# Kernel optimization log

Measured on AMD Instinct MI355X. Metric: run time of the kernel, lower is better.

Reference implementation:

```python
import jax, jax.numpy as jnp
import numpy as np

B, T, N = 128, 4096, 48  # batch, seq_len, num NER tags


def setup_inputs() -> dict:
    key = jax.random.key(0)
    k1, k2, k3, k4, k5 = jax.random.split(key, 5)
    return {
        "emissions": jax.random.normal(k1, (B, T, N), dtype=jnp.float32) * 0.01,
        "transitions": jax.random.normal(k2, (N, N), dtype=jnp.float32) * 0.01,
        "start": jax.random.normal(k3, (N,), dtype=jnp.float32) * 0.01,
        "end": jax.random.normal(k4, (N,), dtype=jnp.float32) * 0.01,
        "tags": jax.random.randint(k5, (B, T), 0, N, dtype=jnp.int32),
    }


def _crf_nll(emissions, transitions, start, end, tags):
    # --- forward_partition: log Z via forward algorithm (logsumexp recursion) ---
    em_t = jnp.transpose(emissions, (1, 0, 2))  # [T, B, N]
    alpha0 = start[None, :] + em_t[0]           # dp[0][j] = start(j) + emit(0, j)

    def step(alpha, em):
        # alpha: [B, N] over previous tag y_; transitions[y_, y]
        new = jax.nn.logsumexp(alpha[:, :, None] + transitions[None, :, :], axis=1) + em
        return new, None

    alpha_T, _ = jax.lax.scan(step, alpha0, em_t[1:])  # [B, N]
    log_Z = jax.nn.logsumexp(alpha_T + end[None, :], axis=-1)  # [B]

    # --- score_seq: gold-path score ---
    em_score = jnp.take_along_axis(emissions, tags[:, :, None], axis=2)[:, :, 0].sum(axis=1)
    trans_score = transitions[tags[:, :-1], tags[:, 1:]].sum(axis=1)
    score = start[tags[:, 0]] + em_score + trans_score + end[tags[:, -1]]

    return log_Z - score  # per-sequence NLL, [B]


def reference(emissions, transitions, start, end, tags):
    return _crf_nll(emissions, transitions, start, end, tags)
```

## Files before the change

### kernel.cpp

```cpp
#include <hip/hip_runtime.h>
#include <cmath>

#define BB 128
#define TT 4096
#define NN 48

typedef short bf16x8 __attribute__((ext_vector_type(8)));
typedef float f32x4 __attribute__((ext_vector_type(4)));
typedef float v2f   __attribute__((ext_vector_type(2)));
typedef int   i32x4 __attribute__((ext_vector_type(4)));
typedef int   i32x2 __attribute__((ext_vector_type(2)));

__device__ __forceinline__ float wave_reduce_sum(float v) {
  #pragma unroll
  for (int m = 32; m >= 1; m >>= 1) v += __shfl_xor(v, m, 64);
  return v;
}
__device__ __forceinline__ int bperm(int byteidx, int src) {
  return __builtin_amdgcn_ds_bpermute(byteidx, src);
}
__device__ __forceinline__ float lane_bcast(float x, int lane) {
  return __uint_as_float((unsigned)__builtin_amdgcn_readlane(__float_as_int(x), lane));
}
__device__ __forceinline__ int cvt_pk_bf16(float lo, float hi) {
  int r;
  asm("v_cvt_pk_bf16_f32 %0, %1, %2" : "=v"(r) : "v"(lo), "v"(hi));
  return r;
}
__device__ __forceinline__ unsigned short f2bf(float f) {
  unsigned u = __float_as_uint(f);
  unsigned r = (u + 0x7FFFu + ((u >> 16) & 1u)) >> 16;
  return (unsigned short)r;
}

template<int NC, int CL>
__launch_bounds__(64, 2)
__global__ void crf_chunk_kernel(const float* __restrict__ em,
                                 const float* __restrict__ trans,
                                 const int* __restrict__ tags,
                                 unsigned short* __restrict__ G,
                                 float* __restrict__ sc_part) {
  const int blk = blockIdx.x;
  const int b = blk / NC;
  const int c = blk % NC;
  const int l = threadIdx.x;
  const int g = l >> 4;
  const int rr = l & 15;
  const int jc = (l < NN) ? l : (NN - 1);
  const float FSCALE = 1.0f / 48.0f;

  bf16x8 Af0[3], Af1[3];
  #pragma unroll
  for (int mt = 0; mt < 3; ++mt) {
    const int i = 16 * mt + rr;
    bf16x8 a0, a1;
    #pragma unroll
    for (int e = 0; e < 8; ++e) {
      int k0 = 16 * (e >> 2) + 4 * g + (e & 3);
      a0[e] = (short)f2bf(__expf(trans[k0 * NN + i]) * FSCALE);
      int k1 = 32 + 4 * g + e;
      a1[e] = (e < 4) ? (short)f2bf(__expf(trans[k1 * NN + i]) * FSCALE) : (short)0;
    }
    Af0[mt] = a0; Af1[mt] = a1;
  }

  int pk0[3][3], pk1[3][3];
  #pragma unroll
  for (int mt = 0; mt < 3; ++mt)
  #pragma unroll
  for (int nt = 0; nt < 3; ++nt) {
    int r0 = 16 * mt + 4 * g, col = 16 * nt + rr;
    pk0[mt][nt] = ((r0     == col) ? 0x3F80 : 0) | (((r0 + 1 == col) ? 0x3F80 : 0) << 16);
    pk1[mt][nt] = ((r0 + 2 == col) ? 0x3F80 : 0) | (((r0 + 3 == col) ? 0x3F80 : 0) << 16);
  }

  const float* embr = em + (size_t)b * TT * NN + jc;
  const int t0 = c * CL + 1;
  const int count = (c == NC - 1) ? (CL - 1) : CL;
  const int wbase = g << 4;

  float pf0 = embr[(size_t)(t0 + 0) * NN];
  float pf1 = embr[(size_t)(t0 + 1) * NN];
  float pf2 = embr[(size_t)(t0 + 2) * NN];
  float pf3 = embr[(size_t)(t0 + 3) * NN];

  #define STEP(PF, NEXT_T) do {                                               \
    float w_ = __expf(PF);                                                    \
    int nt_ = (NEXT_T) > (TT - 1) ? (TT - 1) : (NEXT_T);                      \
    PF = embr[(size_t)nt_ * NN];                                              \
    int wi_ = __float_as_int(w_);                                             \
    v2f wv_[3][2];                                                            \
    _Pragma("unroll") for (int mt = 0; mt < 3; ++mt)                          \
    _Pragma("unroll") for (int h = 0; h < 2; ++h) {                           \
      int wa = bperm(wbase + mt * 64 + (2 * h) * 4, wi_);                     \
      int wb = bperm(wbase + mt * 64 + (2 * h + 1) * 4, wi_);                 \
      v2f t; t.x = __uint_as_float((unsigned)wa);                             \
      t.y = __uint_as_float((unsigned)wb); wv_[mt][h] = t;                    \
    }                                                                         \
    i32x4 B0v[3], B1v[3];                                                     \
    _Pragma("unroll") for (int nt = 0; nt < 3; ++nt) {                        \
      i32x4 b0; b0[0]=pk0[0][nt]; b0[1]=pk1[0][nt]; b0[2]=pk0[1][nt]; b0[3]=pk1[1][nt]; \
      i32x4 b1; b1[0]=pk0[2][nt]; b1[1]=pk1[2][nt]; b1[2]=0; b1[3]=0;         \
      B0v[nt] = b0; B1v[nt] = b1;                                             \
    }                                                                         \
    f32x4 acc_[3][3];                                                         \
    _Pragma("unroll") for (int mt = 0; mt < 3; ++mt)                          \
    _Pragma("unroll") for (int nt = 0; nt < 3; ++nt) {                        \
      f32x4 z = {0.f, 0.f, 0.f, 0.f};                                         \
      z = __builtin_amdgcn_mfma_f32_16x16x32_bf16(                            \
            Af0[mt], __builtin_bit_cast(bf16x8, B0v[nt]), z, 0, 0, 0);        \
      z = __builtin_amdgcn_mfma_f32_16x16x32_bf16(                            \
            Af1[mt], __builtin_bit_cast(bf16x8, B1v[nt]), z, 0, 0, 0);        \
      acc_[mt][nt] = z;                                                       \
    }                                                                         \
    _Pragma("unroll") for (int mt = 0; mt < 3; ++mt)                          \
    _Pragma("unroll") for (int nt = 0; nt < 3; ++nt) {                        \
      v2f lo; lo.x = acc_[mt][nt][0]; lo.y = acc_[mt][nt][1];                 \
      v2f hi; hi.x = acc_[mt][nt][2]; hi.y = acc_[mt][nt][3];                 \
      lo = lo * wv_[mt][0]; hi = hi * wv_[mt][1];                             \
      pk0[mt][nt] = cvt_pk_bf16(lo.x, lo.y);                                  \
      pk1[mt][nt] = cvt_pk_bf16(hi.x, hi.y);                                  \
    }                                                                         \
  } while (0)

  int t = t0;
  #pragma unroll 1
  for (int it = 0; it < count / 4; ++it) {
    STEP(pf0, t + 4);
    STEP(pf1, t + 5);
    STEP(pf2, t + 6);
    STEP(pf3, t + 7);
    t += 4;
  }
  if (count & 3) {
    STEP(pf0, TT - 1);
    STEP(pf1, TT - 1);
    STEP(pf2, TT - 1);
  }
  #undef STEP

  unsigned short* Gc = G + (size_t)blk * (NN * NN);
  #pragma unroll
  for (int mt = 0; mt < 3; ++mt)
  #pragma unroll
  for (int nt = 0; nt < 3; ++nt) {
    i32x2 d; d[0] = pk0[mt][nt]; d[1] = pk1[mt][nt];
    *(i32x2*)(Gc + (16 * nt + rr) * NN + 16 * mt + 4 * g) = d;
  }

  const int* tgb = tags + (size_t)b * TT;
  const float* emb = em + (size_t)b * TT * NN;
  float sc = 0.0f;
  const int base = c * (TT / NC);
  #pragma unroll
  for (int q = 0; q < TT / NC; q += 64) {
    int tt = base + q + l;
    int tg = tgb[tt];
    sc += emb[(size_t)tt * NN + tg];
    if (tt > 0) sc += trans[tgb[tt - 1] * NN + tg];
  }
  sc = wave_reduce_sum(sc);
  if (l == 0) sc_part[blk] = sc;
}

template<int NC>
__launch_bounds__(64, 1)
__global__ void crf_combine_kernel(const float* __restrict__ em,
                                   const float* __restrict__ startv,
                                   const float* __restrict__ endv,
                                   const int* __restrict__ tags,
                                   const unsigned short* __restrict__ G,
                                   const float* __restrict__ sc_part,
                                   float* __restrict__ out) {
  const int b = blockIdx.x;
  const int l = threadIdx.x;
  const int jc = (l < NN) ? l : (NN - 1);
  const float* emb = em + (size_t)b * TT * NN;
  const float FSCALE = 1.0f / 48.0f;

  float r = __expf(startv[jc] + emb[jc]);

  #pragma unroll 1
  for (int c = 0; c < NC; ++c) {
    const unsigned short* Gc = G + (size_t)(b * NC + c) * (NN * NN);
    float s0 = 0.f, s1 = 0.f, s2 = 0.f, s3 = 0.f;
    #pragma unroll
    for (int i = 0; i < NN; i += 4) {
      float g0 = __uint_as_float(((unsigned)Gc[(i + 0) * NN + jc]) << 16);
      float g1 = __uint_as_float(((unsigned)Gc[(i + 1) * NN + jc]) << 16);
      float g2 = __uint_as_float(((unsigned)Gc[(i + 2) * NN + jc]) << 16);
      float g3 = __uint_as_float(((unsigned)Gc[(i + 3) * NN + jc]) << 16);
      s0 = fmaf(lane_bcast(r, i + 0), g0, s0);
      s1 = fmaf(lane_bcast(r, i + 1), g1, s1);
      s2 = fmaf(lane_bcast(r, i + 2), g2, s2);
      s3 = fmaf(lane_bcast(r, i + 3), g3, s3);
    }
    r = (s0 + s1) + (s2 + s3);
  }

  float S = wave_reduce_sum((l < NN) ? r * __expf(endv[jc]) : 0.0f);
  float scp = wave_reduce_sum((l < NC) ? sc_part[b * NC + l] : 0.0f);

  if (l == 0) {
    const int* tgb = tags + (size_t)b * TT;
    double K = -log((double)FSCALE);
    double logZ = log((double)S) + 4095.0 * K;
    double score = (double)scp + (double)startv[tgb[0]] + (double)endv[tgb[TT - 1]];
    out[b] = (float)(logZ - score);
  }
}

extern "C" void kernel_launch(void* const* d_in, const int* in_sizes, int n_in,
                              void* d_out, int out_size, void* d_ws, size_t ws_size,
                              hipStream_t stream) {
  const float* em     = (const float*)d_in[0];
  const float* trans  = (const float*)d_in[1];
  const float* startv = (const float*)d_in[2];
  const float* endv   = (const float*)d_in[3];
  const int*   tags   = (const int*)d_in[4];
  float* out = (float*)d_out;

  const size_t need32 = (size_t)BB * 32 * NN * NN * 2 + (size_t)BB * 32 * 4;
  if (ws_size >= need32) {
    constexpr int NC = 32, CL = TT / 32;
    unsigned short* G = (unsigned short*)d_ws;
    float* sc_part = (float*)((char*)d_ws + (size_t)BB * NC * NN * NN * 2);
    hipLaunchKernelGGL((crf_chunk_kernel<NC, CL>), dim3(BB * NC), dim3(64), 0, stream,
                       em, trans, tags, G, sc_part);
    hipLaunchKernelGGL((crf_combine_kernel<NC>), dim3(BB), dim3(64), 0, stream,
                       em, startv, endv, tags, G, sc_part, out);
  } else {
    constexpr int NC = 16, CL = TT / 16;
    unsigned short* G = (unsigned short*)d_ws;
    float* sc_part = (float*)((char*)d_ws + (size_t)BB * NC * NN * NN * 2);
    hipLaunchKernelGGL((crf_chunk_kernel<NC, CL>), dim3(BB * NC), dim3(64), 0, stream,
                       em, trans, tags, G, sc_part);
    hipLaunchKernelGGL((crf_combine_kernel<NC>), dim3(BB), dim3(64), 0, stream,
                       em, startv, endv, tags, G, sc_part, out);
  }
}
```

Baseline: 141.4 us.

## Keep MFMA B operands packed in place and deepen emission prefetch to eight

The chunk recurrence now keeps its bf16 state directly in the packed B-operand vectors. This removes the per-step repacking from pk arrays into i32x4, and each column tile's MFMA chain and bf16 conversion is interleaved independently so the three tiles can overlap. Emission prefetch depth and loop unroll go from 4 to 8, and launch bounds ask for 4 waves per SIMD instead of 2. The tradeoff is higher register pressure from the deeper prefetch against the tighter occupancy target, which could cause spills.

```diff
diff --git a/kernel.cpp b/kernel.cpp
--- a/kernel.cpp
+++ b/kernel.cpp
@@ -7,7 +7,6 @@
 
 typedef short bf16x8 __attribute__((ext_vector_type(8)));
 typedef float f32x4 __attribute__((ext_vector_type(4)));
-typedef float v2f   __attribute__((ext_vector_type(2)));
 typedef int   i32x4 __attribute__((ext_vector_type(4)));
 typedef int   i32x2 __attribute__((ext_vector_type(2)));
 
@@ -34,7 +33,7 @@
 }
 
 template<int NC, int CL>
-__launch_bounds__(64, 2)
+__launch_bounds__(64, 4)
 __global__ void crf_chunk_kernel(const float* __restrict__ em,
                                  const float* __restrict__ trans,
                                  const int* __restrict__ tags,
@@ -64,88 +63,104 @@
     Af0[mt] = a0; Af1[mt] = a1;
   }
 
-  int pk0[3][3], pk1[3][3];
-  #pragma unroll
-  for (int mt = 0; mt < 3; ++mt)
+  i32x4 B0s[3], B1s[3];
   #pragma unroll
   for (int nt = 0; nt < 3; ++nt) {
-    int r0 = 16 * mt + 4 * g, col = 16 * nt + rr;
-    pk0[mt][nt] = ((r0     == col) ? 0x3F80 : 0) | (((r0 + 1 == col) ? 0x3F80 : 0) << 16);
-    pk1[mt][nt] = ((r0 + 2 == col) ? 0x3F80 : 0) | (((r0 + 3 == col) ? 0x3F80 : 0) << 16);
-  }
+    const int col = 16 * nt + rr;
+    i32x4 b0, b1;
+    #pragma unroll
+    for (int w = 0; w < 4; ++w) {
+      int r0 = 16 * (w >> 1) + 4 * g + 2 * (w & 1);
+      b0[w] = ((r0 == col) ? 0x3F80 : 0) | (((r0 + 1 == col) ? 0x3F80 : 0) << 16);
+    }
+    b1[0] = ((32 + 4 * g == col) ? 0x3F80 : 0) | (((33 + 4 * g == col) ? 0x3F80 : 0) << 16);
+    b1[1] = ((34 + 4 * g == col) ? 0x3F80 : 0) | (((35 + 4 * g == col) ? 0x3F80 : 0) << 16);
+    b1[2] = 0; b1[3] = 0;
+    B0s[nt] = b0; B1s[nt] = b1;
+  }
+
+  const f32x4 zq = {0.f, 0.f, 0.f, 0.f};
 
   const float* embr = em + (size_t)b * TT * NN + jc;
   const int t0 = c * CL + 1;
   const int count = (c == NC - 1) ? (CL - 1) : CL;
-  const int wbase = g << 4;
+  const int wbyte = g << 4;
 
   float pf0 = embr[(size_t)(t0 + 0) * NN];
   float pf1 = embr[(size_t)(t0 + 1) * NN];
   float pf2 = embr[(size_t)(t0 + 2) * NN];
   float pf3 = embr[(size_t)(t0 + 3) * NN];
+  float pf4 = embr[(size_t)(t0 + 4) * NN];
+  float pf5 = embr[(size_t)(t0 + 5) * NN];
+  float pf6 = embr[(size_t)(t0 + 6) * NN];
+  float pf7 = embr[(size_t)(t0 + 7) * NN];
 
   #define STEP(PF, NEXT_T) do {                                               \
     float w_ = __expf(PF);                                                    \
-    int nt_ = (NEXT_T) > (TT - 1) ? (TT - 1) : (NEXT_T);                      \
-    PF = embr[(size_t)nt_ * NN];                                              \
+    int nxt_ = (NEXT_T) > (TT - 1) ? (TT - 1) : (NEXT_T);                     \
+    PF = embr[(size_t)nxt_ * NN];                                             \
     int wi_ = __float_as_int(w_);                                             \
-    v2f wv_[3][2];                                                            \
+    float wb_[12];                                                            \
     _Pragma("unroll") for (int mt = 0; mt < 3; ++mt)                          \
-    _Pragma("unroll") for (int h = 0; h < 2; ++h) {                           \
-      int wa = bperm(wbase + mt * 64 + (2 * h) * 4, wi_);                     \
-      int wb = bperm(wbase + mt * 64 + (2 * h + 1) * 4, wi_);                 \
-      v2f t; t.x = __uint_as_float((unsigned)wa);                             \
-      t.y = __uint_as_float((unsigned)wb); wv_[mt][h] = t;                    \
-    }                                                                         \
-    i32x4 B0v[3], B1v[3];                                                     \
+    _Pragma("unroll") for (int r = 0; r < 4; ++r)                             \
+      wb_[mt * 4 + r] =                                                       \
+          __uint_as_float((unsigned)bperm(wbyte + mt * 64 + r * 4, wi_));     \
     _Pragma("unroll") for (int nt = 0; nt < 3; ++nt) {                        \
-      i32x4 b0; b0[0]=pk0[0][nt]; b0[1]=pk1[0][nt]; b0[2]=pk0[1][nt]; b0[3]=pk1[1][nt]; \
-      i32x4 b1; b1[0]=pk0[2][nt]; b1[1]=pk1[2][nt]; b1[2]=0; b1[3]=0;         \
-      B0v[nt] = b0; B1v[nt] = b1;                                             \
-    }                                                                         \
-    f32x4 acc_[3][3];                                                         \
-    _Pragma("unroll") for (int mt = 0; mt < 3; ++mt)                          \
-    _Pragma("unroll") for (int nt = 0; nt < 3; ++nt) {                        \
-      f32x4 z = {0.f, 0.f, 0.f, 0.f};                                         \
-      z = __builtin_amdgcn_mfma_f32_16x16x32_bf16(                            \
-            Af0[mt], __builtin_bit_cast(bf16x8, B0v[nt]), z, 0, 0, 0);        \
-      z = __builtin_amdgcn_mfma_f32_16x16x32_bf16(                            \
-            Af1[mt], __builtin_bit_cast(bf16x8, B1v[nt]), z, 0, 0, 0);        \
-      acc_[mt][nt] = z;                                                       \
-    }                                                                         \
-    _Pragma("unroll") for (int mt = 0; mt < 3; ++mt)                          \
-    _Pragma("unroll") for (int nt = 0; nt < 3; ++nt) {                        \
-      v2f lo; lo.x = acc_[mt][nt][0]; lo.y = acc_[mt][nt][1];                 \
-      v2f hi; hi.x = acc_[mt][nt][2]; hi.y = acc_[mt][nt][3];                 \
-      lo = lo * wv_[mt][0]; hi = hi * wv_[mt][1];                             \
-      pk0[mt][nt] = cvt_pk_bf16(lo.x, lo.y);                                  \
-      pk1[mt][nt] = cvt_pk_bf16(hi.x, hi.y);                                  \
+      f32x4 a0_ = __builtin_amdgcn_mfma_f32_16x16x32_bf16(                    \
+          Af0[0], __builtin_bit_cast(bf16x8, B0s[nt]), zq, 0, 0, 0);          \
+      f32x4 a1_ = __builtin_amdgcn_mfma_f32_16x16x32_bf16(                    \
+          Af0[1], __builtin_bit_cast(bf16x8, B0s[nt]), zq, 0, 0, 0);          \
+      f32x4 a2_ = __builtin_amdgcn_mfma_f32_16x16x32_bf16(                    \
+          Af0[2], __builtin_bit_cast(bf16x8, B0s[nt]), zq, 0, 0, 0);          \
+      a0_ = __builtin_amdgcn_mfma_f32_16x16x32_bf16(                          \
+          Af1[0], __builtin_bit_cast(bf16x8, B1s[nt]), a0_, 0, 0, 0);         \
+      a1_ = __builtin_amdgcn_mfma_f32_16x16x32_bf16(                          \
+          Af1[1], __builtin_bit_cast(bf16x8, B1s[nt]), a1_, 0, 0, 0);         \
+      a2_ = __builtin_amdgcn_mfma_f32_16x16x32_bf16(                          \
+          Af1[2], __builtin_bit_cast(bf16x8, B1s[nt]), a2_, 0, 0, 0);         \
+      B0s[nt][0] = cvt_pk_bf16(a0_[0] * wb_[0],  a0_[1] * wb_[1]);            \
+      B0s[nt][1] = cvt_pk_bf16(a0_[2] * wb_[2],  a0_[3] * wb_[3]);            \
+      B0s[nt][2] = cvt_pk_bf16(a1_[0] * wb_[4],  a1_[1] * wb_[5]);            \
+      B0s[nt][3] = cvt_pk_bf16(a1_[2] * wb_[6],  a1_[3] * wb_[7]);            \
+      B1s[nt][0] = cvt_pk_bf16(a2_[0] * wb_[8],  a2_[1] * wb_[9]);            \
+      B1s[nt][1] = cvt_pk_bf16(a2_[2] * wb_[10], a2_[3] * wb_[11]);           \
     }                                                                         \
   } while (0)
 
   int t = t0;
   #pragma unroll 1
-  for (int it = 0; it < count / 4; ++it) {
-    STEP(pf0, t + 4);
-    STEP(pf1, t + 5);
-    STEP(pf2, t + 6);
-    STEP(pf3, t + 7);
-    t += 4;
-  }
-  if (count & 3) {
+  for (int it = 0; it < count / 8; ++it) {
+    STEP(pf0, t + 8);
+    STEP(pf1, t + 9);
+    STEP(pf2, t + 10);
+    STEP(pf3, t + 11);
+    STEP(pf4, t + 12);
+    STEP(pf5, t + 13);
+    STEP(pf6, t + 14);
+    STEP(pf7, t + 15);
+    t += 8;
+  }
+  if (count & 7) {
     STEP(pf0, TT - 1);
     STEP(pf1, TT - 1);
     STEP(pf2, TT - 1);
+    STEP(pf3, TT - 1);
+    STEP(pf4, TT - 1);
+    STEP(pf5, TT - 1);
+    STEP(pf6, TT - 1);
   }
   #undef STEP
 
   unsigned short* Gc = G + (size_t)blk * (NN * NN);
   #pragma unroll
-  for (int mt = 0; mt < 3; ++mt)
-  #pragma unroll
   for (int nt = 0; nt < 3; ++nt) {
-    i32x2 d; d[0] = pk0[mt][nt]; d[1] = pk1[mt][nt];
-    *(i32x2*)(Gc + (16 * nt + rr) * NN + 16 * mt + 4 * g) = d;
+    const int rowoff = (16 * nt + rr) * NN + 4 * g;
+    i32x2 d0; d0[0] = B0s[nt][0]; d0[1] = B0s[nt][1];
+    i32x2 d1; d1[0] = B0s[nt][2]; d1[1] = B0s[nt][3];
+    i32x2 d2; d2[0] = B1s[nt][0]; d2[1] = B1s[nt][1];
+    *(i32x2*)(Gc + rowoff)      = d0;
+    *(i32x2*)(Gc + rowoff + 16) = d1;
+    *(i32x2*)(Gc + rowoff + 32) = d2;
   }
 
   const int* tgb = tags + (size_t)b * TT;
```

Result: faster. 136.4 us (-3.5%).
